# Performance work log

Hardware: AMD Instinct MI355X
Metric: run time of the kernel (lower is better)

The kernel has to match this reference:

```python
import jax, jax.numpy as jnp
import numpy as np

B, T, F, H, FW = 4096, 200, 32, 8, 5  # batch, seq, features, hidden, forward_size


def setup_inputs() -> dict:
    key = jax.random.key(0)
    ks = jax.random.split(key, 12)
    s_ih = 1.0 / np.sqrt(F + 1)
    s_hh = 1.0 / np.sqrt(H)
    inp = {
        "x": jax.random.normal(ks[0], (B, T, F), dtype=jnp.float32),
        "z0": jax.random.uniform(ks[1], (1, B, 1), dtype=jnp.float32),
        # LSTM cell over concat([x_t, z_{t-1}]) -> hidden 8, torch gate order i,f,g,o
        "W_ih": jax.random.uniform(ks[2], (4 * H, F + 1), minval=-s_ih, maxval=s_ih),
        "W_hh": jax.random.uniform(ks[3], (4 * H, H), minval=-s_hh, maxval=s_hh),
        "b_ih": jax.random.uniform(ks[4], (4 * H,), minval=-s_hh, maxval=s_hh),
        "b_hh": jax.random.uniform(ks[5], (4 * H,), minval=-s_hh, maxval=s_hh),
        # forward head: 8 -> 5 (relu, dropout inert at inference) -> 1 (relu, monotone increment)
        "W1": jax.random.uniform(ks[6], (FW, H), minval=-s_hh, maxval=s_hh),
        "b1": jax.random.uniform(ks[7], (FW,), minval=-s_hh, maxval=s_hh),
        "W2": jax.random.uniform(ks[8], (1, FW), minval=-1 / np.sqrt(FW), maxval=1 / np.sqrt(FW)),
        "b2": jax.random.uniform(ks[9], (1,), minval=-1 / np.sqrt(FW), maxval=1 / np.sqrt(FW)),
    }
    return inp


def _monotonic_lstm(x, z0, W_ih, W_hh, b_ih, b_hh, W1, b1, W2, b2):
    Bloc = x.shape[0]
    h0 = jnp.zeros((Bloc, H), x.dtype)
    c0 = jnp.zeros((Bloc, H), x.dtype)
    z = z0[0]  # (B, 1) : drop num_layers dim
    bias = b_ih + b_hh

    def step(carry, xt):
        h, c, z = carry
        inp = jnp.concatenate([xt, z], axis=-1)  # (B, F+1)
        gates = inp @ W_ih.T + h @ W_hh.T + bias  # (B, 4H)
        i, f, g, o = jnp.split(gates, 4, axis=-1)
        c = jax.nn.sigmoid(f) * c + jax.nn.sigmoid(i) * jnp.tanh(g)
        h = jax.nn.sigmoid(o) * jnp.tanh(c)
        d = jax.nn.relu(h @ W1.T + b1)            # dropout is identity at inference
        delta = jax.nn.relu(d @ W2.T + b2)        # nonnegative increment -> monotone z
        z = z + delta
        return (h, c, z), z

    _, zs = jax.lax.scan(step, (h0, c0, z), jnp.swapaxes(x, 0, 1))  # zs: (T, B, 1)
    return jnp.swapaxes(zs, 0, 1)  # (B, T, 1)


def reference(x, z0, W_ih, W_hh, b_ih, b_hh, W1, b1, W2, b2):
    return _monotonic_lstm(x, z0, W_ih, W_hh, b_ih, b_hh, W1, b1, W2, b2)
```

## Files before the change

### kernel.cpp

```cpp
#include <hip/hip_runtime.h>

#define T_LEN 200
#define F_IN  32
#define TC    8
#define NCH   (T_LEN / TC)
#define PSTR  264
#define ZSTR  204

#define QP(a,b,c,d) ((a)|((b)<<2)|((c)<<4)|((d)<<6))
#define DPP_HM 0x141

typedef short  bf16x8  __attribute__((ext_vector_type(8)));
typedef float  floatx4 __attribute__((ext_vector_type(4)));

template <int CTRL>
__device__ __forceinline__ float dppf(float v) {
    return __int_as_float(__builtin_amdgcn_update_dpp(
        0, __float_as_int(v), CTRL, 0xF, 0xF, true));
}
__device__ __forceinline__ void bfsplit(float x, short& hi, short& lo) {
    unsigned u = __float_as_uint(x);
    unsigned short h = (unsigned short)(u >> 16);
    float fh = __uint_as_float(((unsigned)h) << 16);
    float r  = x - fh;
    hi = (short)h;
    lo = (short)(__float_as_uint(r) >> 16);
}

__launch_bounds__(128, 1)
__global__ void mono_lstm_kernel(const float* __restrict__ x,
                                 const float* __restrict__ z0,
                                 const float* __restrict__ W_ih,
                                 const float* __restrict__ W_hh,
                                 const float* __restrict__ b_ih,
                                 const float* __restrict__ b_hh,
                                 const float* __restrict__ W1,
                                 const float* __restrict__ b1,
                                 const float* __restrict__ W2,
                                 const float* __restrict__ b2,
                                 float* __restrict__ out) {
    __shared__ float pls[2 * 8 * PSTR];
    __shared__ float zls[8 * ZSTR];

    const int tid  = threadIdx.x;
    const int lane = tid & 63;
    const int wv   = tid >> 6;
    const int bl   = lane >> 3;
    const int j    = lane & 7;
    const int bg   = blockIdx.x * 8;

    const float L2E = 1.4426950408889634f;
    const float NSC = -L2E;
    const float NSG = -2.0f * L2E;

    const int n  = lane & 15;
    const int kq = lane >> 4;
    bf16x8 Bh0, Bl0, Bh1, Bl1;
    float bias0 = 0.f, bias1 = 0.f;

    const int   am  = lane & 15;
    const float* xa = x + ((size_t)(bg + (am >> 1)) * T_LEN + (am & 1)) * F_IN + kq * 8;

    float4 rgv[8];
    auto load_x = [&](int ch) {
#pragma unroll
        for (int s = 0; s < 4; ++s) {
            const float* p = xa + (size_t)(ch * TC + 2 * s) * F_IN;
            rgv[2 * s]     = *(const float4*)p;
            rgv[2 * s + 1] = *(const float4*)(p + 4);
        }
    };
    auto mfma_phase = [&](int buf) {
#pragma unroll
        for (int s = 0; s < 4; ++s) {
            const float xv[8] = {rgv[2*s].x, rgv[2*s].y, rgv[2*s].z, rgv[2*s].w,
                                 rgv[2*s+1].x, rgv[2*s+1].y, rgv[2*s+1].z, rgv[2*s+1].w};
            bf16x8 Ah, Al;
#pragma unroll
            for (int i = 0; i < 8; ++i) {
                short h, l;
                bfsplit(xv[i], h, l);
                Ah[i] = h; Al[i] = l;
            }
            floatx4 a0 = {bias0, bias0, bias0, bias0};
            floatx4 a1 = {bias1, bias1, bias1, bias1};
            a0 = __builtin_amdgcn_mfma_f32_16x16x32_bf16(Ah, Bh0, a0, 0, 0, 0);
            a0 = __builtin_amdgcn_mfma_f32_16x16x32_bf16(Al, Bh0, a0, 0, 0, 0);
            a0 = __builtin_amdgcn_mfma_f32_16x16x32_bf16(Ah, Bl0, a0, 0, 0, 0);
            a1 = __builtin_amdgcn_mfma_f32_16x16x32_bf16(Ah, Bh1, a1, 0, 0, 0);
            a1 = __builtin_amdgcn_mfma_f32_16x16x32_bf16(Al, Bh1, a1, 0, 0, 0);
            a1 = __builtin_amdgcn_mfma_f32_16x16x32_bf16(Ah, Bl1, a1, 0, 0, 0);
#pragma unroll
            for (int reg = 0; reg < 4; ++reg) {
                const int mr = (lane >> 4) * 4 + reg;
                const int bb = mr >> 1, tt = 2 * s + (mr & 1);
                pls[buf * 8 * PSTR + bb * PSTR + tt * 32 + n]      = a0[reg];
                pls[buf * 8 * PSTR + bb * PSTR + tt * 32 + 16 + n] = a1[reg];
            }
        }
    };

    float whi[8], whf[8], whg[8], who[8];
    float wzi = 0.f, wzf = 0.f, wzg = 0.f, wzo = 0.f;
    float w1h[5][8], b1v[5], w2v[5];
    float b2v = 0.f;
    float ha0 = 0.f, ha1 = 0.f, ha2 = 0.f, ha3 = 0.f,
          ha4 = 0.f, ha5 = 0.f, ha6 = 0.f, ha7 = 0.f;
    float c = 0.0f;
    float z = 0.f;

    if (wv == 1) {
        const int row0 = n, row1 = 16 + n;
        const float sc0 = NSC;
        const float sc1 = (n < 8) ? NSG : NSC;
#pragma unroll
        for (int i = 0; i < 8; ++i) {
            const int k = kq * 8 + i;
            short h, l;
            bfsplit(W_ih[row0 * 33 + k] * sc0, h, l); Bh0[i] = h; Bl0[i] = l;
            bfsplit(W_ih[row1 * 33 + k] * sc1, h, l); Bh1[i] = h; Bl1[i] = l;
        }
        bias0 = (b_ih[row0] + b_hh[row0]) * sc0;
        bias1 = (b_ih[row1] + b_hh[row1]) * sc1;

        load_x(0);
        mfma_phase(0);
        load_x(1);
    } else {
        const int ri = j, rf = 8 + j, rg_ = 16 + j, ro = 24 + j;
#pragma unroll
        for (int k = 0; k < 8; ++k) {
            whi[k] = W_hh[ri * 8 + (j ^ k)] * NSC;
            whf[k] = W_hh[rf * 8 + (j ^ k)] * NSC;
            whg[k] = W_hh[rg_ * 8 + (j ^ k)] * NSG;
            who[k] = W_hh[ro * 8 + (j ^ k)] * NSC;
        }
        wzi = W_ih[ri * 33 + 32] * NSC;
        wzf = W_ih[rf * 33 + 32] * NSC;
        wzg = W_ih[rg_ * 33 + 32] * NSG;
        wzo = W_ih[ro * 33 + 32] * NSC;

#pragma unroll
        for (int m = 0; m < 5; ++m) {
#pragma unroll
            for (int k = 0; k < 8; ++k) w1h[m][k] = W1[m * 8 + (j ^ k)];
            b1v[m] = b1[m];
            w2v[m] = W2[m];
        }
        b2v = b2[0];
        z = z0[bg + bl];
    }

    __syncthreads();

    for (int ch = 0; ch < NCH; ++ch) {
        if (wv == 1) {
            if (ch + 1 < NCH) {
                mfma_phase((ch + 1) & 1);
                if (ch + 2 < NCH) load_x(ch + 2);
            }
        } else {
            const int base = (ch & 1) * 8 * PSTR + bl * PSTR;
            float pvi[TC], pvf[TC], pvg[TC], pvo[TC];
#pragma unroll
            for (int t = 0; t < TC; ++t) {
                pvi[t] = pls[base + t * 32 + j];
                pvf[t] = pls[base + t * 32 + 8 + j];
                pvg[t] = pls[base + t * 32 + 16 + j];
                pvo[t] = pls[base + t * 32 + 24 + j];
            }

#pragma unroll
            for (int t = 0; t < TC; ++t) {
                float mi = fmaf(whi[0], ha0, fmaf(whi[1], ha1,
                           fmaf(whi[2], ha2, fmaf(whi[3], ha3, pvi[t]))));
                float ni = fmaf(whi[4], ha4, fmaf(whi[5], ha5,
                           fmaf(whi[6], ha6, whi[7] * ha7)));
                float mf = fmaf(whf[0], ha0, fmaf(whf[1], ha1,
                           fmaf(whf[2], ha2, fmaf(whf[3], ha3, pvf[t]))));
                float nf = fmaf(whf[4], ha4, fmaf(whf[5], ha5,
                           fmaf(whf[6], ha6, whf[7] * ha7)));
                float mg = fmaf(whg[0], ha0, fmaf(whg[1], ha1,
                           fmaf(whg[2], ha2, fmaf(whg[3], ha3, pvg[t]))));
                float ng = fmaf(whg[4], ha4, fmaf(whg[5], ha5,
                           fmaf(whg[6], ha6, whg[7] * ha7)));
                float mo = fmaf(who[0], ha0, fmaf(who[1], ha1,
                           fmaf(who[2], ha2, fmaf(who[3], ha3, pvo[t]))));
                float no = fmaf(who[4], ha4, fmaf(who[5], ha5,
                           fmaf(who[6], ha6, who[7] * ha7)));

                const float ai = fmaf(wzi, z, mi + ni);
                const float af = fmaf(wzf, z, mf + nf);
                const float ag = fmaf(wzg, z, mg + ng);
                const float ao = fmaf(wzo, z, mo + no);

                const float si = __builtin_amdgcn_rcpf(1.0f + __builtin_amdgcn_exp2f(ai));
                const float sf = __builtin_amdgcn_rcpf(1.0f + __builtin_amdgcn_exp2f(af));
                const float sg = __builtin_amdgcn_rcpf(1.0f + __builtin_amdgcn_exp2f(ag));
                const float so = __builtin_amdgcn_rcpf(1.0f + __builtin_amdgcn_exp2f(ao));
                const float tg = fmaf(2.0f, sg, -1.0f);

                c = fmaf(sf, c, si * tg);
                const float ec = __builtin_amdgcn_exp2f(c * (-2.0f * L2E));
                const float tc = fmaf(2.0f, __builtin_amdgcn_rcpf(1.0f + ec), -1.0f);
                const float hn = so * tc;

                ha0 = hn;
                ha1 = dppf<QP(1, 0, 3, 2)>(hn);
                ha2 = dppf<QP(2, 3, 0, 1)>(hn);
                ha3 = dppf<QP(3, 2, 1, 0)>(hn);
                const float t7 = dppf<DPP_HM>(hn);
                ha7 = t7;
                ha4 = dppf<QP(3, 2, 1, 0)>(t7);
                ha5 = dppf<QP(2, 3, 0, 1)>(t7);
                ha6 = dppf<QP(1, 0, 3, 2)>(t7);

                float d0a = fmaf(w1h[0][0], ha0, fmaf(w1h[0][1], ha1, fmaf(w1h[0][2], ha2, b1v[0])));
                float d0b = fmaf(w1h[0][4], ha4, fmaf(w1h[0][5], ha5, fmaf(w1h[0][6], ha6, w1h[0][7] * ha7)));
                float d1a = fmaf(w1h[1][0], ha0, fmaf(w1h[1][1], ha1, fmaf(w1h[1][2], ha2, b1v[1])));
                float d1b = fmaf(w1h[1][4], ha4, fmaf(w1h[1][5], ha5, fmaf(w1h[1][6], ha6, w1h[1][7] * ha7)));
                float d2a = fmaf(w1h[2][0], ha0, fmaf(w1h[2][1], ha1, fmaf(w1h[2][2], ha2, b1v[2])));
                float d2b = fmaf(w1h[2][4], ha4, fmaf(w1h[2][5], ha5, fmaf(w1h[2][6], ha6, w1h[2][7] * ha7)));
                float d3a = fmaf(w1h[3][0], ha0, fmaf(w1h[3][1], ha1, fmaf(w1h[3][2], ha2, b1v[3])));
                float d3b = fmaf(w1h[3][4], ha4, fmaf(w1h[3][5], ha5, fmaf(w1h[3][6], ha6, w1h[3][7] * ha7)));
                float d4a = fmaf(w1h[4][0], ha0, fmaf(w1h[4][1], ha1, fmaf(w1h[4][2], ha2, b1v[4])));
                float d4b = fmaf(w1h[4][4], ha4, fmaf(w1h[4][5], ha5, fmaf(w1h[4][6], ha6, w1h[4][7] * ha7)));
                const float d0 = fmaxf(fmaf(w1h[0][3], ha3, d0a + d0b), 0.0f);
                const float d1 = fmaxf(fmaf(w1h[1][3], ha3, d1a + d1b), 0.0f);
                const float d2 = fmaxf(fmaf(w1h[2][3], ha3, d2a + d2b), 0.0f);
                const float d3 = fmaxf(fmaf(w1h[3][3], ha3, d3a + d3b), 0.0f);
                const float d4 = fmaxf(fmaf(w1h[4][3], ha3, d4a + d4b), 0.0f);
                const float q1 = fmaf(w2v[0], d0, fmaf(w2v[1], d1, b2v));
                const float q2 = fmaf(w2v[2], d2, fmaf(w2v[3], d3, w2v[4] * d4));
                z += fmaxf(q1 + q2, 0.0f);

                if (j == t) zls[bl * ZSTR + ch * TC + t] = z;
            }
        }
        __syncthreads();
    }

#pragma unroll
    for (int it = 0; it < 4; ++it) {
        const int idx = tid + it * 128;
        if (idx < 8 * (T_LEN / 4)) {
            const int bb = idx / 50, rem = idx - bb * 50;
            *(float4*)&out[(size_t)(bg + bb) * T_LEN + rem * 4] =
                *(const float4*)&zls[bb * ZSTR + rem * 4];
        }
    }
}

extern "C" void kernel_launch(void* const* d_in, const int* in_sizes, int n_in,
                              void* d_out, int out_size, void* d_ws, size_t ws_size,
                              hipStream_t stream) {
    const float* x    = (const float*)d_in[0];
    const float* z0   = (const float*)d_in[1];
    const float* W_ih = (const float*)d_in[2];
    const float* W_hh = (const float*)d_in[3];
    const float* b_ih = (const float*)d_in[4];
    const float* b_hh = (const float*)d_in[5];
    const float* W1   = (const float*)d_in[6];
    const float* b1   = (const float*)d_in[7];
    const float* W2   = (const float*)d_in[8];
    const float* b2   = (const float*)d_in[9];
    float* out = (float*)d_out;

    const int B = in_sizes[1];
    dim3 grid(B / 8), block(128);
    hipLaunchKernelGGL(mono_lstm_kernel, grid, block, 0, stream,
                       x, z0, W_ih, W_hh, b_ih, b_hh, W1, b1, W2, b2, out);
}
```

Measured before the change: 191.8 us.

## Triple-buffer MFMA projections and prefetch next chunk into registers before recurrence

Moves the input-projection staging from double to triple buffering, so the MFMA wave runs two chunks ahead. The recurrence wave now loads the next chunk's projections from LDS into registers while it computes the current chunk, hiding LDS latency. It also rescales the cell state so the tanh/sigmoid algebra saves a few multiplies per step, and stores z once per chunk from a register instead of writing conditionally every step. The costs are more LDS, more registers for the two projection buffers, and code duplicated across the two branches.

```diff
diff --git a/kernel.cpp b/kernel.cpp
--- a/kernel.cpp
+++ b/kernel.cpp
@@ -4,6 +4,7 @@
 #define F_IN  32
 #define TC    8
 #define NCH   (T_LEN / TC)
+#define NB    8
 #define PSTR  264
 #define ZSTR  204
 
@@ -26,6 +27,79 @@
     hi = (short)h;
     lo = (short)(__float_as_uint(r) >> 16);
 }
+
+#define LOADPV(PL, LB)                                                      \
+    do {                                                                    \
+        _Pragma("unroll")                                                   \
+        for (int _t = 0; _t < TC; ++_t) {                                   \
+            const int _a = (LB) + _t * 32 + j;                              \
+            PL[0][_t] = pls[_a];      PL[1][_t] = pls[_a + 8];              \
+            PL[2][_t] = pls[_a + 16]; PL[3][_t] = pls[_a + 24];             \
+        }                                                                   \
+    } while (0)
+
+#define HUNIT(m)                                                            \
+    fmaxf((fmaf(w1h[m][2], ha2, fmaf(w1h[m][1], ha1, fmaf(w1h[m][0], ha0, b1v[m]))) \
+         + fmaf(w1h[m][5], ha5, fmaf(w1h[m][4], ha4, w1h[m][3] * ha3)))     \
+         + fmaf(w1h[m][7], ha7, w1h[m][6] * ha6), 0.0f)
+
+#define STEP8(PU)                                                           \
+    do {                                                                    \
+        _Pragma("unroll")                                                   \
+        for (int t = 0; t < TC; ++t) {                                      \
+            float mi = fmaf(whi[0], ha0, fmaf(whi[1], ha1,                  \
+                       fmaf(whi[2], ha2, fmaf(whi[3], ha3, PU[0][t]))));    \
+            float ni = fmaf(whi[4], ha4, fmaf(whi[5], ha5,                  \
+                       fmaf(whi[6], ha6, whi[7] * ha7)));                   \
+            float mf = fmaf(whf[0], ha0, fmaf(whf[1], ha1,                  \
+                       fmaf(whf[2], ha2, fmaf(whf[3], ha3, PU[1][t]))));    \
+            float nf = fmaf(whf[4], ha4, fmaf(whf[5], ha5,                  \
+                       fmaf(whf[6], ha6, whf[7] * ha7)));                   \
+            float mg = fmaf(whg[0], ha0, fmaf(whg[1], ha1,                  \
+                       fmaf(whg[2], ha2, fmaf(whg[3], ha3, PU[2][t]))));    \
+            float ng = fmaf(whg[4], ha4, fmaf(whg[5], ha5,                  \
+                       fmaf(whg[6], ha6, whg[7] * ha7)));                   \
+            float mo = fmaf(who[0], ha0, fmaf(who[1], ha1,                  \
+                       fmaf(who[2], ha2, fmaf(who[3], ha3, PU[3][t]))));    \
+            float no = fmaf(who[4], ha4, fmaf(who[5], ha5,                  \
+                       fmaf(who[6], ha6, who[7] * ha7)));                   \
+            const float ai = fmaf(wzi, z, mi + ni);                         \
+            const float af = fmaf(wzf, z, mf + nf);                         \
+            const float ag = fmaf(wzg, z, mg + ng);                         \
+            const float ao = fmaf(wzo, z, mo + no);                         \
+            const float si = __builtin_amdgcn_rcpf(1.0f + __builtin_amdgcn_exp2f(ai)); \
+            const float sf = __builtin_amdgcn_rcpf(1.0f + __builtin_amdgcn_exp2f(af)); \
+            const float sg = __builtin_amdgcn_rcpf(1.0f + __builtin_amdgcn_exp2f(ag)); \
+            const float so = __builtin_amdgcn_rcpf(1.0f + __builtin_amdgcn_exp2f(ao)); \
+             \
+            const float si2K  = si * C2K;                                   \
+            const float msiK  = si * CPK;                                   \
+            const float prodk = fmaf(si2K, sg, msiK);                       \
+            ck = fmaf(sf, ck, prodk);                                       \
+            const float ec  = __builtin_amdgcn_exp2f(ck);                   \
+            const float rc  = __builtin_amdgcn_rcpf(1.0f + ec);             \
+            const float so2 = so + so;                                      \
+            const float hn  = fmaf(so2, rc, -so);           \
+            ha0 = hn;                                                       \
+            ha1 = dppf<QP(1, 0, 3, 2)>(hn);                                 \
+            ha2 = dppf<QP(2, 3, 0, 1)>(hn);                                 \
+            ha3 = dppf<QP(3, 2, 1, 0)>(hn);                                 \
+            const float t7 = dppf<DPP_HM>(hn);                              \
+            ha7 = t7;                                                       \
+            ha4 = dppf<QP(3, 2, 1, 0)>(t7);                                 \
+            ha5 = dppf<QP(2, 3, 0, 1)>(t7);                                 \
+            ha6 = dppf<QP(1, 0, 3, 2)>(t7);                                 \
+            const float d0 = HUNIT(0);                                      \
+            const float d1 = HUNIT(1);                                      \
+            const float d2 = HUNIT(2);                                      \
+            const float d3 = HUNIT(3);                                      \
+            const float d4 = HUNIT(4);                                      \
+            const float q1 = fmaf(w2v[1], d1, fmaf(w2v[0], d0, b2v));       \
+            const float q2 = fmaf(w2v[2], d2, fmaf(w2v[3], d3, w2v[4] * d4)); \
+            z += fmaxf(q1 + q2, 0.0f);                                      \
+            zk = (j == t) ? z : zk;                                         \
+        }                                                                   \
+    } while (0)
 
 __launch_bounds__(128, 1)
 __global__ void mono_lstm_kernel(const float* __restrict__ x,
@@ -39,19 +113,21 @@
                                  const float* __restrict__ W2,
                                  const float* __restrict__ b2,
                                  float* __restrict__ out) {
-    __shared__ float pls[2 * 8 * PSTR];
-    __shared__ float zls[8 * ZSTR];
+    __shared__ float pls[3 * NB * PSTR];
+    __shared__ float zls[NB * ZSTR];
 
     const int tid  = threadIdx.x;
     const int lane = tid & 63;
     const int wv   = tid >> 6;
     const int bl   = lane >> 3;
     const int j    = lane & 7;
-    const int bg   = blockIdx.x * 8;
+    const int bg   = blockIdx.x * NB;
 
     const float L2E = 1.4426950408889634f;
     const float NSC = -L2E;
     const float NSG = -2.0f * L2E;
+    const float C2K = -4.0f * L2E;
+    const float CPK =  2.0f * L2E;
 
     const int n  = lane & 15;
     const int kq = lane >> 4;
@@ -94,8 +170,8 @@
             for (int reg = 0; reg < 4; ++reg) {
                 const int mr = (lane >> 4) * 4 + reg;
                 const int bb = mr >> 1, tt = 2 * s + (mr & 1);
-                pls[buf * 8 * PSTR + bb * PSTR + tt * 32 + n]      = a0[reg];
-                pls[buf * 8 * PSTR + bb * PSTR + tt * 32 + 16 + n] = a1[reg];
+                pls[buf * NB * PSTR + bb * PSTR + tt * 32 + n]      = a0[reg];
+                pls[buf * NB * PSTR + bb * PSTR + tt * 32 + 16 + n] = a1[reg];
             }
         }
     };
@@ -106,8 +182,10 @@
     float b2v = 0.f;
     float ha0 = 0.f, ha1 = 0.f, ha2 = 0.f, ha3 = 0.f,
           ha4 = 0.f, ha5 = 0.f, ha6 = 0.f, ha7 = 0.f;
-    float c = 0.0f;
-    float z = 0.f;
+    float ck = 0.0f;
+    float z  = 0.f;
+    float zk = 0.f;
+    float pvA[4][8], pvB[4][8];
 
     if (wv == 1) {
         const int row0 = n, row1 = 16 + n;
@@ -126,6 +204,8 @@
         load_x(0);
         mfma_phase(0);
         load_x(1);
+        mfma_phase(1);
+        load_x(2);
     } else {
         const int ri = j, rf = 8 + j, rg_ = 16 + j, ro = 24 + j;
 #pragma unroll
@@ -153,97 +233,34 @@
 
     __syncthreads();
 
+    if (wv == 0) {
+        const int lb0 = bl * PSTR;
+        LOADPV(pvA, lb0);
+    }
+
+    int rb0 = 0, rb1 = 1, rb2 = 2;
     for (int ch = 0; ch < NCH; ++ch) {
         if (wv == 1) {
+            if (ch + 2 < NCH) {
+                mfma_phase(rb2);
+                if (ch + 3 < NCH) load_x(ch + 3);
+            }
+        } else {
             if (ch + 1 < NCH) {
-                mfma_phase((ch + 1) & 1);
-                if (ch + 2 < NCH) load_x(ch + 2);
-            }
-        } else {
-            const int base = (ch & 1) * 8 * PSTR + bl * PSTR;
-            float pvi[TC], pvf[TC], pvg[TC], pvo[TC];
-#pragma unroll
-            for (int t = 0; t < TC; ++t) {
-                pvi[t] = pls[base + t * 32 + j];
-                pvf[t] = pls[base + t * 32 + 8 + j];
-                pvg[t] = pls[base + t * 32 + 16 + j];
-                pvo[t] = pls[base + t * 32 + 24 + j];
-            }
-
-#pragma unroll
-            for (int t = 0; t < TC; ++t) {
-                float mi = fmaf(whi[0], ha0, fmaf(whi[1], ha1,
-                           fmaf(whi[2], ha2, fmaf(whi[3], ha3, pvi[t]))));
-                float ni = fmaf(whi[4], ha4, fmaf(whi[5], ha5,
-                           fmaf(whi[6], ha6, whi[7] * ha7)));
-                float mf = fmaf(whf[0], ha0, fmaf(whf[1], ha1,
-                           fmaf(whf[2], ha2, fmaf(whf[3], ha3, pvf[t]))));
-                float nf = fmaf(whf[4], ha4, fmaf(whf[5], ha5,
-                           fmaf(whf[6], ha6, whf[7] * ha7)));
-                float mg = fmaf(whg[0], ha0, fmaf(whg[1], ha1,
-                           fmaf(whg[2], ha2, fmaf(whg[3], ha3, pvg[t]))));
-                float ng = fmaf(whg[4], ha4, fmaf(whg[5], ha5,
-                           fmaf(whg[6], ha6, whg[7] * ha7)));
-                float mo = fmaf(who[0], ha0, fmaf(who[1], ha1,
-                           fmaf(who[2], ha2, fmaf(who[3], ha3, pvo[t]))));
-                float no = fmaf(who[4], ha4, fmaf(who[5], ha5,
-                           fmaf(who[6], ha6, who[7] * ha7)));
-
-                const float ai = fmaf(wzi, z, mi + ni);
-                const float af = fmaf(wzf, z, mf + nf);
-                const float ag = fmaf(wzg, z, mg + ng);
-                const float ao = fmaf(wzo, z, mo + no);
-
-                const float si = __builtin_amdgcn_rcpf(1.0f + __builtin_amdgcn_exp2f(ai));
-                const float sf = __builtin_amdgcn_rcpf(1.0f + __builtin_amdgcn_exp2f(af));
-                const float sg = __builtin_amdgcn_rcpf(1.0f + __builtin_amdgcn_exp2f(ag));
-                const float so = __builtin_amdgcn_rcpf(1.0f + __builtin_amdgcn_exp2f(ao));
-                const float tg = fmaf(2.0f, sg, -1.0f);
-
-                c = fmaf(sf, c, si * tg);
-                const float ec = __builtin_amdgcn_exp2f(c * (-2.0f * L2E));
-                const float tc = fmaf(2.0f, __builtin_amdgcn_rcpf(1.0f + ec), -1.0f);
-                const float hn = so * tc;
-
-                ha0 = hn;
-                ha1 = dppf<QP(1, 0, 3, 2)>(hn);
-                ha2 = dppf<QP(2, 3, 0, 1)>(hn);
-                ha3 = dppf<QP(3, 2, 1, 0)>(hn);
-                const float t7 = dppf<DPP_HM>(hn);
-                ha7 = t7;
-                ha4 = dppf<QP(3, 2, 1, 0)>(t7);
-                ha5 = dppf<QP(2, 3, 0, 1)>(t7);
-                ha6 = dppf<QP(1, 0, 3, 2)>(t7);
-
-                float d0a = fmaf(w1h[0][0], ha0, fmaf(w1h[0][1], ha1, fmaf(w1h[0][2], ha2, b1v[0])));
-                float d0b = fmaf(w1h[0][4], ha4, fmaf(w1h[0][5], ha5, fmaf(w1h[0][6], ha6, w1h[0][7] * ha7)));
-                float d1a = fmaf(w1h[1][0], ha0, fmaf(w1h[1][1], ha1, fmaf(w1h[1][2], ha2, b1v[1])));
-                float d1b = fmaf(w1h[1][4], ha4, fmaf(w1h[1][5], ha5, fmaf(w1h[1][6], ha6, w1h[1][7] * ha7)));
-                float d2a = fmaf(w1h[2][0], ha0, fmaf(w1h[2][1], ha1, fmaf(w1h[2][2], ha2, b1v[2])));
-                float d2b = fmaf(w1h[2][4], ha4, fmaf(w1h[2][5], ha5, fmaf(w1h[2][6], ha6, w1h[2][7] * ha7)));
-                float d3a = fmaf(w1h[3][0], ha0, fmaf(w1h[3][1], ha1, fmaf(w1h[3][2], ha2, b1v[3])));
-                float d3b = fmaf(w1h[3][4], ha4, fmaf(w1h[3][5], ha5, fmaf(w1h[3][6], ha6, w1h[3][7] * ha7)));
-                float d4a = fmaf(w1h[4][0], ha0, fmaf(w1h[4][1], ha1, fmaf(w1h[4][2], ha2, b1v[4])));
-                float d4b = fmaf(w1h[4][4], ha4, fmaf(w1h[4][5], ha5, fmaf(w1h[4][6], ha6, w1h[4][7] * ha7)));
-                const float d0 = fmaxf(fmaf(w1h[0][3], ha3, d0a + d0b), 0.0f);
-                const float d1 = fmaxf(fmaf(w1h[1][3], ha3, d1a + d1b), 0.0f);
-                const float d2 = fmaxf(fmaf(w1h[2][3], ha3, d2a + d2b), 0.0f);
-                const float d3 = fmaxf(fmaf(w1h[3][3], ha3, d3a + d3b), 0.0f);
-                const float d4 = fmaxf(fmaf(w1h[4][3], ha3, d4a + d4b), 0.0f);
-                const float q1 = fmaf(w2v[0], d0, fmaf(w2v[1], d1, b2v));
-                const float q2 = fmaf(w2v[2], d2, fmaf(w2v[3], d3, w2v[4] * d4));
-                z += fmaxf(q1 + q2, 0.0f);
-
-                if (j == t) zls[bl * ZSTR + ch * TC + t] = z;
-            }
+                const int lb = rb1 * NB * PSTR + bl * PSTR;
+                if (ch & 1) { LOADPV(pvA, lb); } else { LOADPV(pvB, lb); }
+            }
+            if (ch & 1) { STEP8(pvB); } else { STEP8(pvA); }
+            zls[bl * ZSTR + ch * TC + j] = zk;
         }
         __syncthreads();
+        const int rr = rb0; rb0 = rb1; rb1 = rb2; rb2 = rr;
     }
 
 #pragma unroll
     for (int it = 0; it < 4; ++it) {
         const int idx = tid + it * 128;
-        if (idx < 8 * (T_LEN / 4)) {
+        if (idx < NB * (T_LEN / 4)) {
             const int bb = idx / 50, rem = idx - bb * 50;
             *(float4*)&out[(size_t)(bg + bb) * T_LEN + rem * 4] =
                 *(const float4*)&zls[bb * ZSTR + rem * 4];
@@ -267,7 +284,7 @@
     float* out = (float*)d_out;
 
     const int B = in_sizes[1];
-    dim3 grid(B / 8), block(128);
+    dim3 grid(B / NB), block(128);
     hipLaunchKernelGGL(mono_lstm_kernel, grid, block, 0, stream,
                        x, z0, W_ih, W_hh, b_ih, b_hh, W1, b1, W2, b2, out);
 }
```

Result: no change. 194.0 us (+1.2%).
